# Optimization experiments

Hardware: AMD Instinct MI355X
Metric: run time of the kernel (lower is better)

The kernel has to match this reference:

```python
import jax, jax.numpy as jnp
import numpy as np

B, T, N, D = 32, 24, 325, 64
NUM_HEADS = 8


def setup_inputs() -> dict:
    key = jax.random.key(0)
    ks = jax.random.split(key, 8)
    s = 0.02
    return {
        "X": jax.random.normal(ks[0], (B, T, N, D), dtype=jnp.float32),
        "STE": jax.random.normal(ks[1], (B, T, N, D), dtype=jnp.float32),
        "Wq": jax.random.normal(ks[2], (D, D), dtype=jnp.float32) * s,
        "bq": jnp.zeros((D,), dtype=jnp.float32),
        "Wk": jax.random.normal(ks[3], (D, D), dtype=jnp.float32) * s,
        "bk": jnp.zeros((D,), dtype=jnp.float32),
        "Wv": jax.random.normal(ks[4], (D, D), dtype=jnp.float32) * s,
        "bv": jnp.zeros((D,), dtype=jnp.float32),
        "Wf1": jax.random.normal(ks[5], (D, D), dtype=jnp.float32) * s,
        "bf1": jnp.zeros((D,), dtype=jnp.float32),
        "Wf2": jax.random.normal(ks[6], (D, D), dtype=jnp.float32) * s,
        "bf2": jnp.zeros((D,), dtype=jnp.float32),
        "K": 8,
        "d": 8,
        "bn_decay": 0,
    }


def reference(X, STE, Wq, bq, Wk, bk, Wv, bv, Wf1, bf1, Wf2, bf2, K, d, bn_decay):
    # FC projections (1x1 linear + ReLU), matching FC(emb_size, units=D, act=ReLU)
    q = jax.nn.relu(X @ Wq + bq)  # [B,T,N,D]
    k = jax.nn.relu(X @ Wk + bk)
    v = jax.nn.relu(X @ Wv + bv)
    b, t, n, dm = q.shape
    dh = dm // K  # head dim == d
    # chunk(K, dim=-1) + cat(dim=0) == split D into K heads (head k <- feature block k)
    qh = q.reshape(b, t, n, K, dh)
    kh = k.reshape(b, t, n, K, dh)
    vh = v.reshape(b, t, n, K, dh)
    # scores over temporal axis per (batch, head, node): [B,K,N,T,T]
    attn = jnp.einsum('btnkd,bsnkd->bknts', qh, kh) / jnp.sqrt(jnp.float32(d))
    # upper-triangular (incl. diagonal) kept, rest filled with -2**15 + 1
    tri = jnp.triu(jnp.ones((t, t), dtype=bool))
    attn = jnp.where(tri, attn, jnp.float32(-2 ** 15 + 1))
    attn = jax.nn.softmax(attn, axis=-1)
    out = jnp.einsum('bknts,bsnkd->btnkd', attn, vh).reshape(b, t, n, dm)
    # output FC: [D -> D (ReLU) -> D (linear)]
    h = jax.nn.relu(out @ Wf1 + bf1)
    return h @ Wf2 + bf2
```

## Files before the change

kernel.cpp:

```cpp
#include <hip/hip_runtime.h>
#include <hip/hip_bf16.h>

#define BB 32
#define TT 24
#define NN 325
#define DD 64
#define RSH 72
#define RSF 68

typedef _Float16 h4 __attribute__((ext_vector_type(4)));
typedef _Float16 h2 __attribute__((ext_vector_type(2)));
typedef float    f4 __attribute__((ext_vector_type(4)));

__global__ void prep_w_kernel(const float* __restrict__ Wq, const float* __restrict__ Wk,
                              const float* __restrict__ Wv, const float* __restrict__ Wf1,
                              const float* __restrict__ Wf2, _Float16* __restrict__ Wt)
{
    __shared__ float tile[64][65];
    const float* W;
    switch (blockIdx.x) {
        case 0: W = Wq; break;
        case 1: W = Wk; break;
        case 2: W = Wv; break;
        case 3: W = Wf1; break;
        default: W = Wf2; break;
    }
    const int tid = threadIdx.x;
    const int g = tid >> 6, c = tid & 63;
    #pragma unroll
    for (int p = 0; p < 16; ++p) {
        const int row = p * 4 + g;
        tile[row][c] = W[row * 64 + c];
    }
    __syncthreads();
    _Float16* dst = Wt + blockIdx.x * 4096;
    #pragma unroll
    for (int p = 0; p < 16; ++p) {
        const int col = p * 4 + g;
        dst[col * 64 + c] = (_Float16)tile[c][col];
    }
}

__device__ inline float dot8(h4 qa, h4 qb, h4 ka, h4 kb) {
#if __has_builtin(__builtin_amdgcn_fdot2)
    h2 qa0 = {qa[0], qa[1]}, qa1 = {qa[2], qa[3]};
    h2 qb0 = {qb[0], qb[1]}, qb1 = {qb[2], qb[3]};
    h2 ka0 = {ka[0], ka[1]}, ka1 = {ka[2], ka[3]};
    h2 kb0 = {kb[0], kb[1]}, kb1 = {kb[2], kb[3]};
    float d = __builtin_amdgcn_fdot2(qa0, ka0, 0.f, false);
    d = __builtin_amdgcn_fdot2(qa1, ka1, d, false);
    d = __builtin_amdgcn_fdot2(qb0, kb0, d, false);
    d = __builtin_amdgcn_fdot2(qb1, kb1, d, false);
    return d;
#else
    return (float)qa[0]*(float)ka[0] + (float)qa[1]*(float)ka[1]
         + (float)qa[2]*(float)ka[2] + (float)qa[3]*(float)ka[3]
         + (float)qb[0]*(float)kb[0] + (float)qb[1]*(float)kb[1]
         + (float)qb[2]*(float)kb[2] + (float)qb[3]*(float)kb[3];
#endif
}

__global__ __launch_bounds__(128) void ta_wave_kernel(
    const float* __restrict__ X, const _Float16* __restrict__ Wt,
    const float* __restrict__ bq, const float* __restrict__ bk,
    const float* __restrict__ bv, const float* __restrict__ bf1,
    const float* __restrict__ bf2, float* __restrict__ Out)
{
    const int wid  = threadIdx.x >> 6;
    const int lane = threadIdx.x & 63;
    const int gw = blockIdx.x * 2 + wid;
    const int b = gw / NN, n = gw - b * NN;
    const int lr = lane & 15, lg = lane >> 4;

    __shared__ _Float16 qsh[2][TT * RSH];
    __shared__ _Float16 ksh[2][TT * RSH];
    __shared__ float    vsh[2][TT * RSF];
    _Float16* q = qsh[wid];
    _Float16* k = ksh[wid];
    float*    v = vsh[wid];

    const size_t xbase = (((size_t)b * TT) * NN + n) * DD;

    h4 a[2][4];
    #pragma unroll
    for (int mt = 0; mt < 2; ++mt) {
        const int row = mt * 16 + lr;
        const bool ok = row < TT;
        const float* xp = X + xbase + (size_t)row * (NN * DD);
        #pragma unroll
        for (int kt = 0; kt < 4; ++kt) {
            f4 x = {0.f, 0.f, 0.f, 0.f};
            if (ok) x = *(const f4*)(xp + kt * 16 + lg * 4);
            h4 h;
            h[0] = (_Float16)x[0]; h[1] = (_Float16)x[1];
            h[2] = (_Float16)x[2]; h[3] = (_Float16)x[3];
            a[mt][kt] = h;
        }
    }

#define MATMUL_NT(WOFF, BIASP, STORE)                                            \
    {                                                                            \
        _Pragma("unroll")                                                        \
        for (int nt = 0; nt < 4; ++nt) {                                         \
            const int col = 16 * nt + lr;                                        \
            const _Float16* wp = Wt + (WOFF) + col * 64 + lg * 4;                \
            h4 bfr[4];                                                           \
            _Pragma("unroll")                                                    \
            for (int kt = 0; kt < 4; ++kt) bfr[kt] = *(const h4*)(wp + kt * 16); \
            const float bb = (BIASP)[col];                                       \
            f4 acc0 = {bb, bb, bb, bb};                                          \
            f4 acc1 = acc0;                                                      \
            _Pragma("unroll")                                                    \
            for (int kt = 0; kt < 4; ++kt) {                                     \
                acc0 = __builtin_amdgcn_mfma_f32_16x16x16f16(a[0][kt], bfr[kt], acc0, 0, 0, 0); \
                acc1 = __builtin_amdgcn_mfma_f32_16x16x16f16(a[1][kt], bfr[kt], acc1, 0, 0, 0); \
            }                                                                    \
            _Pragma("unroll")                                                    \
            for (int r = 0; r < 4; ++r) {                                        \
                const int row0 = 4 * lg + r;                                     \
                const int row1 = 16 + row0;                                      \
                STORE(row0, col, acc0[r]);                                       \
                if (row1 < TT) STORE(row1, col, acc1[r]);                        \
            }                                                                    \
        }                                                                        \
    }

#define STQ(rr, cc, vv) q[(rr) * RSH + (cc)] = (_Float16)fmaxf((vv), 0.f)
#define STK(rr, cc, vv) k[(rr) * RSH + (cc)] = (_Float16)fmaxf((vv), 0.f)
#define STV(rr, cc, vv) v[(rr) * RSF + (cc)] = fmaxf((vv), 0.f)
#define STH(rr, cc, vv) k[(rr) * RSH + (cc)] = (_Float16)fmaxf((vv), 0.f)
#define STO(rr, cc, vv) Out[xbase + (size_t)(rr) * (NN * DD) + (cc)] = (vv)

#define LOAD_AFRAG(SRC)                                                          \
    {                                                                            \
        _Pragma("unroll")                                                        \
        for (int mt = 0; mt < 2; ++mt) {                                         \
            const int row = 16 * mt + lr;                                        \
            _Pragma("unroll")                                                    \
            for (int kt = 0; kt < 4; ++kt) {                                     \
                h4 tmpf = {(_Float16)0, (_Float16)0, (_Float16)0, (_Float16)0};  \
                if (row < TT) tmpf = *(const h4*)&(SRC)[row * RSH + kt * 16 + lg * 4]; \
                a[mt][kt] = tmpf;                                                \
            }                                                                    \
        }                                                                        \
    }

    MATMUL_NT(0 * 4096, bq, STQ)
    MATMUL_NT(1 * 4096, bk, STK)
    MATMUL_NT(2 * 4096, bv, STV)

    {
        const int kh = lane & 7;
        const int tl = lane >> 3;
        #pragma unroll
        for (int p = 0; p < 3; ++p) {
            const int t = 8 * p + tl;
            const h4 qa = *(const h4*)&q[t * RSH + kh * 8];
            const h4 qb = *(const h4*)&q[t * RSH + kh * 8 + 4];
            float sc[TT];
            float mx = -3.0e38f;
            #pragma unroll
            for (int s = 8 * p; s < TT; ++s) {
                const h4 ka = *(const h4*)&k[s * RSH + kh * 8];
                const h4 kb = *(const h4*)&k[s * RSH + kh * 8 + 4];
                float d = dot8(qa, qb, ka, kb) * 0.35355339059327373f;
                d = (s >= t) ? d : -3.0e38f;
                sc[s] = d;
                mx = fmaxf(mx, d);
            }
            float sum = 0.f;
            #pragma unroll
            for (int s = 8 * p; s < TT; ++s) {
                const float e = __expf(sc[s] - mx);
                sc[s] = e;
                sum += e;
            }
            f4 oa = {0.f, 0.f, 0.f, 0.f}, ob = {0.f, 0.f, 0.f, 0.f};
            #pragma unroll
            for (int s = 8 * p; s < TT; ++s) {
                const f4 va = *(const f4*)&v[s * RSF + kh * 8];
                const f4 vb = *(const f4*)&v[s * RSF + kh * 8 + 4];
                const float pp = sc[s];
                oa += pp * va;
                ob += pp * vb;
            }
            const float inv = 1.f / sum;
            h4 ha, hb;
            #pragma unroll
            for (int i = 0; i < 4; ++i) {
                ha[i] = (_Float16)(oa[i] * inv);
                hb[i] = (_Float16)(ob[i] * inv);
            }
            *(h4*)&q[t * RSH + kh * 8]     = ha;
            *(h4*)&q[t * RSH + kh * 8 + 4] = hb;
        }
    }

    LOAD_AFRAG(q)
    MATMUL_NT(3 * 4096, bf1, STH)

    LOAD_AFRAG(k)
    MATMUL_NT(4 * 4096, bf2, STO)
}

extern "C" void kernel_launch(void* const* d_in, const int* in_sizes, int n_in,
                              void* d_out, int out_size, void* d_ws, size_t ws_size,
                              hipStream_t stream) {
    const float* X   = (const float*)d_in[0];
    const float* Wq  = (const float*)d_in[2];
    const float* bq  = (const float*)d_in[3];
    const float* Wk  = (const float*)d_in[4];
    const float* bk  = (const float*)d_in[5];
    const float* Wv  = (const float*)d_in[6];
    const float* bv  = (const float*)d_in[7];
    const float* Wf1 = (const float*)d_in[8];
    const float* bf1 = (const float*)d_in[9];
    const float* Wf2 = (const float*)d_in[10];
    const float* bf2 = (const float*)d_in[11];
    float* Out = (float*)d_out;

    _Float16* Wt = (_Float16*)d_ws;

    prep_w_kernel<<<5, 256, 0, stream>>>(Wq, Wk, Wv, Wf1, Wf2, Wt);
    ta_wave_kernel<<<(BB * NN) / 2, 128, 0, stream>>>(X, Wt, bq, bk, bv, bf1, bf2, Out);
}
```

Before: 270.5 us.

## Split fused attention kernel into QKV, attention and FFN kernels via workspace

Replaces the single fused per-(batch,node) kernel with three kernels. The first does the QKV projection with MFMA over row tiles and writes fp16 Q/K/V to the workspace. The second computes causal temporal attention per (batch,node), and the third runs the two-layer output FFN with MFMA. The aim is better parallelism and coalescing for the GEMM stages than the per-node fused layout gave. In exchange, the fp16 intermediates now make extra round trips through global memory, and the old fused kernel is kept as a fallback when the workspace is too small.

```diff
diff --git a/kernel.cpp b/kernel.cpp
--- a/kernel.cpp
+++ b/kernel.cpp
@@ -5,8 +5,11 @@
 #define TT 24
 #define NN 325
 #define DD 64
+#define MROWS (BB * TT * NN)
+#define BNCNT (BB * NN)
 #define RSH 72
 #define RSF 68
+#define HS  76
 
 typedef _Float16 h4 __attribute__((ext_vector_type(4)));
 typedef _Float16 h2 __attribute__((ext_vector_type(2)));
@@ -58,6 +61,172 @@
          + (float)qb[0]*(float)kb[0] + (float)qb[1]*(float)kb[1]
          + (float)qb[2]*(float)kb[2] + (float)qb[3]*(float)kb[3];
 #endif
+}
+
+__global__ __launch_bounds__(256) void qkv_kernel(
+    const float* __restrict__ X, const _Float16* __restrict__ Wt,
+    const float* __restrict__ bq, const float* __restrict__ bk,
+    const float* __restrict__ bv, _Float16* __restrict__ QKV)
+{
+    const int lane = threadIdx.x & 63, w = threadIdx.x >> 6;
+    const int lr = lane & 15, lg = lane >> 4;
+    const int mbase = (blockIdx.x * 4 + w) * 16;
+    const int m = mbase + lr;
+
+    h4 a[4];
+    const float* xp = X + (size_t)m * DD;
+    #pragma unroll
+    for (int kt = 0; kt < 4; ++kt) {
+        const f4 x = *(const f4*)(xp + kt * 16 + lg * 4);
+        h4 h; h[0] = (_Float16)x[0]; h[1] = (_Float16)x[1];
+        h[2] = (_Float16)x[2]; h[3] = (_Float16)x[3];
+        a[kt] = h;
+    }
+
+    const int b   = m / (TT * NN);
+    const int rem = m - b * (TT * NN);
+    const int t   = rem / NN;
+    const int n   = rem - t * NN;
+    const int bn  = b * NN + n;
+
+    #pragma unroll
+    for (int sep = 0; sep < 3; ++sep) {
+        const float* bias = (sep == 0) ? bq : (sep == 1) ? bk : bv;
+        const _Float16* wsep = Wt + sep * 4096;
+        _Float16* osep = QKV + ((size_t)(bn * 3 + sep) * TT + t) * DD;
+        #pragma unroll
+        for (int nt = 0; nt < 4; ++nt) {
+            h4 bfr[4];
+            const _Float16* wp = wsep + (16 * nt + lr) * 64 + 4 * lg;
+            #pragma unroll
+            for (int kt = 0; kt < 4; ++kt) bfr[kt] = *(const h4*)(wp + 16 * kt);
+            f4 acc = *(const f4*)(bias + 16 * nt + 4 * lg);
+            #pragma unroll
+            for (int kt = 0; kt < 4; ++kt)
+                acc = __builtin_amdgcn_mfma_f32_16x16x16f16(bfr[kt], a[kt], acc, 0, 0, 0);
+            h4 o;
+            #pragma unroll
+            for (int i = 0; i < 4; ++i) o[i] = (_Float16)fmaxf(acc[i], 0.f);
+            *(h4*)(osep + 16 * nt + 4 * lg) = o;
+        }
+    }
+}
+
+__global__ __launch_bounds__(256) void attn_kernel(
+    const _Float16* __restrict__ QKV, _Float16* __restrict__ ATT)
+{
+    const int lane = threadIdx.x & 63, w = threadIdx.x >> 6;
+    const int bn = blockIdx.x * 4 + w;
+    const int kh = lane & 7, tl = lane >> 3;
+
+    const _Float16* qp = QKV + (size_t)(bn * 3 + 0) * TT * DD;
+    const _Float16* kp = QKV + (size_t)(bn * 3 + 1) * TT * DD;
+    const _Float16* vp = QKV + (size_t)(bn * 3 + 2) * TT * DD;
+    const int b = bn / NN, n = bn - b * NN;
+
+    #pragma unroll
+    for (int p = 0; p < 3; ++p) {
+        const int t = 8 * p + tl;
+        const h4 qa = *(const h4*)(qp + t * DD + kh * 8);
+        const h4 qb = *(const h4*)(qp + t * DD + kh * 8 + 4);
+        float sc[TT];
+        float mx = -3.0e38f;
+        #pragma unroll
+        for (int s = 8 * p; s < TT; ++s) {
+            const h4 ka  = *(const h4*)(kp + s * DD + kh * 8);
+            const h4 kb2 = *(const h4*)(kp + s * DD + kh * 8 + 4);
+            float d = dot8(qa, qb, ka, kb2) * 0.35355339059327373f;
+            d = (s >= t) ? d : -3.0e38f;
+            sc[s] = d;
+            mx = fmaxf(mx, d);
+        }
+        float sum = 0.f;
+        #pragma unroll
+        for (int s = 8 * p; s < TT; ++s) {
+            const float e = __expf(sc[s] - mx);
+            sc[s] = e;
+            sum += e;
+        }
+        f4 oa = {0.f, 0.f, 0.f, 0.f}, ob = {0.f, 0.f, 0.f, 0.f};
+        #pragma unroll
+        for (int s = 8 * p; s < TT; ++s) {
+            const h4 va  = *(const h4*)(vp + s * DD + kh * 8);
+            const h4 vb2 = *(const h4*)(vp + s * DD + kh * 8 + 4);
+            const float pp = sc[s];
+            const f4 vaf = {(float)va[0],  (float)va[1],  (float)va[2],  (float)va[3]};
+            const f4 vbf = {(float)vb2[0], (float)vb2[1], (float)vb2[2], (float)vb2[3]};
+            oa += pp * vaf;
+            ob += pp * vbf;
+        }
+        const float inv = 1.f / sum;
+        h4 ha, hb;
+        #pragma unroll
+        for (int i = 0; i < 4; ++i) {
+            ha[i] = (_Float16)(oa[i] * inv);
+            hb[i] = (_Float16)(ob[i] * inv);
+        }
+        _Float16* op = ATT + ((size_t)(b * TT + t) * NN + n) * DD + kh * 8;
+        *(h4*)op       = ha;
+        *(h4*)(op + 4) = hb;
+    }
+}
+
+__global__ __launch_bounds__(256) void ff_kernel(
+    const _Float16* __restrict__ ATT, const _Float16* __restrict__ Wt,
+    const float* __restrict__ bf1, const float* __restrict__ bf2,
+    float* __restrict__ Out)
+{
+    __shared__ _Float16 hbuf[4][16 * HS];
+    const int lane = threadIdx.x & 63, w = threadIdx.x >> 6;
+    const int lr = lane & 15, lg = lane >> 4;
+    const int mbase = (blockIdx.x * 4 + w) * 16;
+    const int m = mbase + lr;
+
+    h4 a[4];
+    const _Float16* ap = ATT + (size_t)m * DD;
+    #pragma unroll
+    for (int kt = 0; kt < 4; ++kt) a[kt] = *(const h4*)(ap + 16 * kt + 4 * lg);
+
+    _Float16* hb = hbuf[w];
+
+    {
+        const _Float16* w1 = Wt + 3 * 4096;
+        #pragma unroll
+        for (int nt = 0; nt < 4; ++nt) {
+            h4 bfr[4];
+            const _Float16* wp = w1 + (16 * nt + lr) * 64 + 4 * lg;
+            #pragma unroll
+            for (int kt = 0; kt < 4; ++kt) bfr[kt] = *(const h4*)(wp + 16 * kt);
+            f4 acc = *(const f4*)(bf1 + 16 * nt + 4 * lg);
+            #pragma unroll
+            for (int kt = 0; kt < 4; ++kt)
+                acc = __builtin_amdgcn_mfma_f32_16x16x16f16(bfr[kt], a[kt], acc, 0, 0, 0);
+            h4 o;
+            #pragma unroll
+            for (int i = 0; i < 4; ++i) o[i] = (_Float16)fmaxf(acc[i], 0.f);
+            *(h4*)(hb + lr * HS + 16 * nt + 4 * lg) = o;
+        }
+    }
+
+    {
+        h4 a2[4];
+        #pragma unroll
+        for (int kt = 0; kt < 4; ++kt)
+            a2[kt] = *(const h4*)(hb + lr * HS + 16 * kt + 4 * lg);
+        const _Float16* w2 = Wt + 4 * 4096;
+        #pragma unroll
+        for (int nt = 0; nt < 4; ++nt) {
+            h4 bfr[4];
+            const _Float16* wp = w2 + (16 * nt + lr) * 64 + 4 * lg;
+            #pragma unroll
+            for (int kt = 0; kt < 4; ++kt) bfr[kt] = *(const h4*)(wp + 16 * kt);
+            f4 acc = *(const f4*)(bf2 + 16 * nt + 4 * lg);
+            #pragma unroll
+            for (int kt = 0; kt < 4; ++kt)
+                acc = __builtin_amdgcn_mfma_f32_16x16x16f16(bfr[kt], a2[kt], acc, 0, 0, 0);
+            *(f4*)(Out + (size_t)m * DD + 16 * nt + 4 * lg) = acc;
+        }
+    }
 }
 
 __global__ __launch_bounds__(128) void ta_wave_kernel(
@@ -198,7 +367,6 @@
 
     LOAD_AFRAG(q)
     MATMUL_NT(3 * 4096, bf1, STH)
-
     LOAD_AFRAG(k)
     MATMUL_NT(4 * 4096, bf2, STO)
 }
@@ -220,7 +388,21 @@
     float* Out = (float*)d_out;
 
     _Float16* Wt = (_Float16*)d_ws;
+    const size_t QKV_OFF   = 65536;
+    const size_t QKV_BYTES = (size_t)BNCNT * 3 * TT * DD * 2;
+    const size_t ATT_OFF   = QKV_OFF + QKV_BYTES;
+    const size_t ATT_BYTES = (size_t)MROWS * DD * 2;
+    const size_t NEED      = ATT_OFF + ATT_BYTES;
 
     prep_w_kernel<<<5, 256, 0, stream>>>(Wq, Wk, Wv, Wf1, Wf2, Wt);
-    ta_wave_kernel<<<(BB * NN) / 2, 128, 0, stream>>>(X, Wt, bq, bk, bv, bf1, bf2, Out);
-}
+
+    if (ws_size >= NEED) {
+        _Float16* QKV = (_Float16*)((char*)d_ws + QKV_OFF);
+        _Float16* ATT = (_Float16*)((char*)d_ws + ATT_OFF);
+        qkv_kernel <<<MROWS / 64, 256, 0, stream>>>(X, Wt, bq, bk, bv, QKV);
+        attn_kernel<<<BNCNT / 4,  256, 0, stream>>>(QKV, ATT);
+        ff_kernel  <<<MROWS / 64, 256, 0, stream>>>(ATT, Wt, bf1, bf2, Out);
+    } else {
+        ta_wave_kernel<<<(BB * NN) / 2, 128, 0, stream>>>(X, Wt, bq, bk, bv, bf1, bf2, Out);
+    }
+}
```

Measured after the change: 385.5 us. 1.43x slower.
